# Optimization experiments

Hardware: AMD Instinct MI355X
Metric: run time of the kernel (lower is better)

The kernel has to match this reference:

```python
import jax, jax.numpy as jnp
from jax import lax
import numpy as np

# dims
N_ENT, M, K = 2048, 64, 32              # entities, mentions, candidates per mention
LT, LB, LM, LC, LD = 32, 128, 16, 128, 512  # char lengths: title, body, mention, context, doc
VOCAB, EMB = 5053, 300
H, HH, CCS, W = 256, 128, 512, 5        # hidden, per-dir LSTM hidden, char channels, conv width


def char_cnn(idx, emb, conv_w, conv_b):
    # Conv2d(1, CCS, [EMB, W]) applied to (N,1,EMB,L) == Conv1d(EMB, CCS, W); relu + max-pool over length
    x = jnp.swapaxes(emb[idx], 1, 2)                        # [N, EMB, L]
    y = lax.conv_general_dilated(x, conv_w, (1,), 'VALID')  # [N, CCS, L-W+1]
    return jax.nn.relu(y + conv_b[None, :, None]).max(axis=2)  # [N, CCS]


def _lstm_dir(x, Wih, Whh, bih, bhh):
    pre = x @ Wih.T + (bih + bhh)                            # [B, T, 4*HH]
    def step(carry, g_t):
        h, c = carry
        i, f, g, o = jnp.split(g_t + h @ Whh.T, 4, axis=-1)
        c = jax.nn.sigmoid(f) * c + jax.nn.sigmoid(i) * jnp.tanh(g)
        h = jax.nn.sigmoid(o) * jnp.tanh(c)
        return (h, c), h
    B = x.shape[0]
    z = jnp.zeros((B, Whh.shape[1]), x.dtype)
    _, hs = lax.scan(step, (z, z), jnp.swapaxes(pre, 0, 1))
    return jnp.swapaxes(hs, 0, 1)


def bilstm(x, Wih_f, Whh_f, bih_f, bhh_f, Wih_b, Whh_b, bih_b, bhh_b):
    fwd = _lstm_dir(x, Wih_f, Whh_f, bih_f, bhh_f)
    bwd = _lstm_dir(x[:, ::-1], Wih_b, Whh_b, bih_b, bhh_b)[:, ::-1]
    return jnp.concatenate([fwd, bwd], axis=-1)              # [B, T, H]


def att_flow(c, q, wc, bc, wq, bq, wcq, bcq):
    # BiDAF attention; c,q: [B,T,H] -> [B,T,4H]
    s = (c @ wc)[:, :, None] + (q @ wq)[:, None, :] \
        + jnp.einsum('bid,bjd,d->bij', c, q, wcq) + (bc + bq + bcq)
    a = jax.nn.softmax(s, axis=2)
    c2q = jnp.einsum('bij,bjd->bid', a, q)
    b = jax.nn.softmax(s.max(axis=2), axis=1)
    q2c = jnp.einsum('bi,bid->bd', b, c)[:, None, :]
    return jnp.concatenate([c, c2q, c * c2q, c * jnp.broadcast_to(q2c, c.shape)], axis=-1)


def setup_inputs() -> dict:
    key = jax.random.key(0)
    ks = jax.random.split(key, 16)
    rng = np.random.RandomState(0)
    # exactly K distinct candidate entities per mention (regularized mention_entity indicator)
    cand_idx = jnp.asarray(np.argsort(rng.rand(M, N_ENT), axis=1)[:, :K])
    emb = jax.random.uniform(ks[0], (VOCAB, EMB), jnp.float32, -0.001, 0.001).at[1].set(0.0)
    def rnd(k, shape, s=0.05):
        return jax.random.normal(k, shape, jnp.float32) * s
    return {
        'title_vec': jax.random.randint(ks[1], (N_ENT, LT), 0, VOCAB),
        'body_vec': jax.random.randint(ks[2], (N_ENT, LB), 0, VOCAB),
        'mention_vec': jax.random.randint(ks[3], (M, LM), 0, VOCAB),
        'context_vec': jax.random.randint(ks[4], (M, LC), 0, VOCAB),
        'doc_vec': jax.random.randint(ks[5], (LD,), 0, VOCAB),
        'cand_idx': cand_idx,
        'emb': emb,
        'conv_w': rnd(ks[6], (CCS, EMB, W), 0.02), 'conv_b': jnp.zeros((CCS,), jnp.float32),
        'Wih_f': rnd(ks[7], (4 * HH, CCS)), 'Whh_f': rnd(ks[8], (4 * HH, HH)),
        'bih_f': jnp.zeros((4 * HH,), jnp.float32), 'bhh_f': jnp.zeros((4 * HH,), jnp.float32),
        'Wih_b': rnd(ks[9], (4 * HH, CCS)), 'Whh_b': rnd(ks[10], (4 * HH, HH)),
        'bih_b': jnp.zeros((4 * HH,), jnp.float32), 'bhh_b': jnp.zeros((4 * HH,), jnp.float32),
        'wc': rnd(ks[11], (H,)), 'bc': jnp.zeros((), jnp.float32),
        'wq': rnd(ks[12], (H,)), 'bq': jnp.zeros((), jnp.float32),
        'wcq': rnd(ks[13], (H,)), 'bcq': jnp.zeros((), jnp.float32),
        'wz': rnd(ks[14], (4 * H,)), 'bz': jnp.zeros((), jnp.float32),
        'w_p1': jnp.asarray(0.7, jnp.float32), 'b_p1': jnp.asarray(0.1, jnp.float32),
        'w_p2': jnp.asarray(0.5, jnp.float32), 'b_p2': jnp.asarray(-0.1, jnp.float32),
    }


def reference(title_vec, body_vec, mention_vec, context_vec, doc_vec, cand_idx,
              emb, conv_w, conv_b,
              Wih_f, Whh_f, bih_f, bhh_f, Wih_b, Whh_b, bih_b, bhh_b,
              wc, bc, wq, bq, wcq, bcq, wz, bz, w_p1, b_p1, w_p2, b_p2):
    m, k = cand_idx.shape
    n = title_vec.shape[0]
    lstm_p = (Wih_f, Whh_f, bih_f, bhh_f, Wih_b, Whh_b, bih_b, bhh_b)
    # char-CNN features (compute once per unique sequence, then gather / broadcast)
    title_feat = char_cnn(title_vec, emb, conv_w, conv_b)         # [n, CCS]
    body_feat = char_cnn(body_vec, emb, conv_w, conv_b)           # [n, CCS]
    ctx_feat = char_cnn(context_vec, emb, conv_w, conv_b)         # [m, CCS]
    doc_feat = char_cnn(doc_vec[None], emb, conv_w, conv_b)[0]    # [CCS]
    # per-mention candidate sequences (seq dim = candidates, as in the original loop)
    title_h = bilstm(title_feat[cand_idx], *lstm_p)               # [m, k, H]
    body_h = bilstm(body_feat[cand_idx], *lstm_p)
    ctx_h = bilstm(jnp.broadcast_to(ctx_feat[:, None, :], (m, k, CCS)), *lstm_p)
    doc_h = bilstm(jnp.broadcast_to(doc_feat[None, None, :], (1, k, CCS)), *lstm_p)
    doc_h = jnp.broadcast_to(doc_h, (m, k, H))
    g = att_flow(ctx_h, title_h, wc, bc, wq, bq, wcq, bcq)        # [m, k, 4H]
    h = att_flow(doc_h, body_h, wc, bc, wq, bq, wcq, bcq)
    p1 = g @ wz + bz                                              # [m, k]
    p2 = h @ wz + bz
    score = w_p1 * p1 + b_p1 + w_p2 * p2 + b_p2
    # len(true_output)==1 branch is always taken in the original: raw scores, softmax, sum-normalized
    score_sm = jax.nn.softmax(score, axis=1)
    score_un = score / score.sum(axis=1, keepdims=True)
    rows = jnp.arange(m)[:, None]
    def scatter(v):
        return jnp.zeros((m, n), v.dtype).at[rows, cand_idx].set(v)
    return scatter(score), scatter(score_sm), scatter(score_un)
```

## Files before the change

kernel.cpp:

```cpp
#include <hip/hip_runtime.h>
#include <hip/hip_fp16.h>
#include <math.h>

#define DEDUP_B 34439168ULL
#define AH_B    34459648ULL
#define BH_B    37695488ULL
#define BHP_B   39333888ULL
#define WHH_B   40382464ULL
#define AHP_B   34459648ULL

typedef _Float16 half8 __attribute__((ext_vector_type(8)));
typedef float f32x4 __attribute__((ext_vector_type(4)));

__device__ inline void add8(float* a, float4 r){
  const __half2* h = (const __half2*)&r;
  #pragma unroll
  for (int q = 0; q < 4; ++q){
    float2 f = __half22float2(h[q]);
    a[2*q]   += f.x;
    a[2*q+1] += f.y;
  }
}

__global__ __launch_bounds__(256) void k_prep(unsigned int* __restrict__ out32, int n,
                                              unsigned int* __restrict__ dd32,
                                              float* __restrict__ featDoc,
                                              const float* __restrict__ emb, _Float16* __restrict__ A_h,
                                              const float* __restrict__ convw, _Float16* __restrict__ B_h,
                                              const float* __restrict__ WihF, const float* __restrict__ WihB,
                                              _Float16* __restrict__ B_hp,
                                              const float* __restrict__ WhhF, const float* __restrict__ WhhB,
                                              _Float16* __restrict__ WhhH){
  const long o0 = n;
  const long o1 = o0 + 2112;
  const long o2 = o1 + 512;
  const long o3 = o2 + 1617920;
  const long o4 = o3 + 819200;
  const long o5 = o4 + 524288;
  const long o6 = o5 + 131072;
  for (long t = (long)blockIdx.x * 256 + threadIdx.x; t < o6; t += (long)gridDim.x * 256){
    if (t < o0){
      out32[t] = 0u;
    } else if (t < o1){
      dd32[t - o0] = 0u;
    } else if (t < o2){
      featDoc[t - o1] = 0.f;
    } else if (t < o3){
      long u = t - o2;
      int row = (int)(u / 320), col = (int)(u - (long)row * 320);
      float v = (row < 5053 && col < 300) ? emb[(size_t)row * 300 + col] * 1024.f : 0.f;
      A_h[u] = (_Float16)v;
    } else if (t < o4){
      long u = t - o3;
      int nn = (int)(u / 320), k = (int)(u - (long)nn * 320);
      int w = nn >> 9, c = nn & 511;
      float v = (k < 300) ? convw[((size_t)c * 300 + k) * 5 + w] : 0.f;
      B_h[u] = (_Float16)v;
    } else if (t < o5){
      long u = t - o4;
      int dir = (int)(u >> 18), r = (int)(u & 262143);
      B_hp[u] = (_Float16)((dir ? WihB : WihF)[r]);
    } else {
      long u = t - o5;
      int dir = (int)(u >> 16), r = (int)(u & 65535);
      WhhH[u] = (_Float16)((dir ? WhhB : WhhF)[r]);
    }
  }
}

__global__ __launch_bounds__(256) void k_mark(const int* __restrict__ cand, int* __restrict__ flags){
  int t = blockIdx.x * 256 + threadIdx.x;
  flags[cand[t]] = 1;
}

__global__ __launch_bounds__(256) void k_compact(const int* __restrict__ flags,
                                                 int* __restrict__ nUsed, int* __restrict__ list){
  int t = blockIdx.x * 256 + threadIdx.x;
  if (flags[t]){
    int s = atomicAdd(nUsed, 1);
    list[s] = t;
  }
}

__global__ __launch_bounds__(256) void k_contrib(const _Float16* __restrict__ A_h,
                                                 const _Float16* __restrict__ B_h,
                                                 __half* __restrict__ contrib){
  int tid = threadIdx.x;
  int lane = tid & 63, wid = tid >> 6;
  int wr = wid >> 1, wc = wid & 1;
  int m0 = blockIdx.x * 64 + wr * 32;
  int n0 = blockIdx.y * 128 + wc * 64;
  int lr = lane & 15, lk = (lane >> 4) * 8;

  const _Float16* Ap = A_h + (size_t)(m0 + lr) * 320 + lk;
  const _Float16* Bp = B_h + (size_t)(n0 + lr) * 320 + lk;

  f32x4 acc[2][4];
  #pragma unroll
  for (int fr = 0; fr < 2; ++fr)
    #pragma unroll
    for (int fc = 0; fc < 4; ++fc) acc[fr][fc] = (f32x4){0.f, 0.f, 0.f, 0.f};

  for (int kk = 0; kk < 320; kk += 32){
    half8 a0 = *(const half8*)(Ap + kk);
    half8 a1 = *(const half8*)(Ap + 16 * 320 + kk);
    half8 b0 = *(const half8*)(Bp + kk);
    half8 b1 = *(const half8*)(Bp + 16 * 320 + kk);
    half8 b2 = *(const half8*)(Bp + 32 * 320 + kk);
    half8 b3 = *(const half8*)(Bp + 48 * 320 + kk);
    acc[0][0] = __builtin_amdgcn_mfma_f32_16x16x32_f16(a0, b0, acc[0][0], 0, 0, 0);
    acc[0][1] = __builtin_amdgcn_mfma_f32_16x16x32_f16(a0, b1, acc[0][1], 0, 0, 0);
    acc[0][2] = __builtin_amdgcn_mfma_f32_16x16x32_f16(a0, b2, acc[0][2], 0, 0, 0);
    acc[0][3] = __builtin_amdgcn_mfma_f32_16x16x32_f16(a0, b3, acc[0][3], 0, 0, 0);
    acc[1][0] = __builtin_amdgcn_mfma_f32_16x16x32_f16(a1, b0, acc[1][0], 0, 0, 0);
    acc[1][1] = __builtin_amdgcn_mfma_f32_16x16x32_f16(a1, b1, acc[1][1], 0, 0, 0);
    acc[1][2] = __builtin_amdgcn_mfma_f32_16x16x32_f16(a1, b2, acc[1][2], 0, 0, 0);
    acc[1][3] = __builtin_amdgcn_mfma_f32_16x16x32_f16(a1, b3, acc[1][3], 0, 0, 0);
  }
  const float s = 1.f / 1024.f;
  #pragma unroll
  for (int fr = 0; fr < 2; ++fr){
    int row = m0 + fr * 16 + (lane >> 4) * 4;
    #pragma unroll
    for (int fc = 0; fc < 4; ++fc){
      int col = n0 + fc * 16 + lr;
      #pragma unroll
      for (int r = 0; r < 4; ++r)
        contrib[(size_t)(row + r) * 2560 + col] = __float2half(acc[fr][fc][r] * s);
    }
  }
}

__global__ __launch_bounds__(256) void k_conv(const int* __restrict__ title_v,
                                              const int* __restrict__ body_v,
                                              const int* __restrict__ ctx_v,
                                              const __half* __restrict__ contrib,
                                              const float* __restrict__ convb,
                                              float* __restrict__ featAll,
                                              const int* __restrict__ list,
                                              const int* __restrict__ nUsed){
  __shared__ int tok[128];
  __shared__ float red[256 * 9];
  int bg = blockIdx.x, tid = threadIdx.x;
  const int* idx; int L, row0; bool useList;
  if (bg < 16384){ idx = title_v; L = 32;  row0 = 0;    useList = true; }
  else if (bg < 32768){ bg -= 16384; idx = body_v; L = 128; row0 = 2048; useList = true; }
  else { bg -= 32768; idx = ctx_v; L = 128; row0 = 4096; useList = false; }
  int g = bg & 7, sIdx = bg >> 3;
  int s = sIdx;
  if (useList){
    if (sIdx >= *nUsed) return;
    s = list[sIdx];
  }
  const int* row = idx + (size_t)s * L;
  for (int i = tid; i < L; i += 256) tok[i] = row[i];
  __syncthreads();
  int c8 = tid & 7;
  int pg = tid >> 3;
  int cOff = g * 64 + c8 * 8;
  float bias[8], mx[8];
  {
    float4 b0 = *(const float4*)(convb + cOff);
    float4 b1 = *(const float4*)(convb + cOff + 4);
    bias[0]=b0.x; bias[1]=b0.y; bias[2]=b0.z; bias[3]=b0.w;
    bias[4]=b1.x; bias[5]=b1.y; bias[6]=b1.z; bias[7]=b1.w;
  }
  #pragma unroll
  for (int k = 0; k < 8; ++k) mx[k] = 0.f;
  int P = L - 4;
  int per = (P + 31) >> 5;
  int p = pg * per, pe = min(p + per, P);
  for (; p + 1 < pe; p += 2){
    float a0[8], a1[8];
    #pragma unroll
    for (int k = 0; k < 8; ++k){ a0[k] = bias[k]; a1[k] = bias[k]; }
    #pragma unroll
    for (int w = 0; w < 5; ++w){
      float4 r0 = *(const float4*)(contrib + ((size_t)tok[p + w] * 5 + w) * 512 + cOff);
      float4 r1 = *(const float4*)(contrib + ((size_t)tok[p + 1 + w] * 5 + w) * 512 + cOff);
      add8(a0, r0);
      add8(a1, r1);
    }
    #pragma unroll
    for (int k = 0; k < 8; ++k) mx[k] = fmaxf(mx[k], fmaxf(a0[k], a1[k]));
  }
  if (p < pe){
    float a0[8];
    #pragma unroll
    for (int k = 0; k < 8; ++k) a0[k] = bias[k];
    #pragma unroll
    for (int w = 0; w < 5; ++w){
      float4 r0 = *(const float4*)(contrib + ((size_t)tok[p + w] * 5 + w) * 512 + cOff);
      add8(a0, r0);
    }
    #pragma unroll
    for (int k = 0; k < 8; ++k) mx[k] = fmaxf(mx[k], a0[k]);
  }
  #pragma unroll
  for (int k = 0; k < 8; ++k) red[tid * 9 + k] = mx[k];
  __syncthreads();
  if (tid < 64){
    int c8r = tid >> 3, kr = tid & 7;
    float o = red[c8r * 9 + kr];
    #pragma unroll
    for (int q = 1; q < 32; ++q)
      o = fmaxf(o, red[(q * 8 + c8r) * 9 + kr]);
    featAll[(size_t)(row0 + s) * 512 + g * 64 + tid] = o;
  }
}

__global__ __launch_bounds__(256) void k_conv_doc(const int* __restrict__ doc,
                                                  const __half* __restrict__ contrib,
                                                  const float* __restrict__ convb,
                                                  float* __restrict__ featDoc){
  __shared__ int tok[512];
  __shared__ float red[256 * 9];
  int b = blockIdx.x, tid = threadIdx.x;
  for (int i = tid; i < 512; i += 256) tok[i] = doc[i];
  __syncthreads();
  int c8 = tid & 63, pg = tid >> 6;
  float bias[8], mx[8];
  {
    float4 b0 = *(const float4*)(convb + c8 * 8);
    float4 b1 = *(const float4*)(convb + c8 * 8 + 4);
    bias[0]=b0.x; bias[1]=b0.y; bias[2]=b0.z; bias[3]=b0.w;
    bias[4]=b1.x; bias[5]=b1.y; bias[6]=b1.z; bias[7]=b1.w;
  }
  #pragma unroll
  for (int k = 0; k < 8; ++k) mx[k] = 0.f;
  int p0 = b * 16, p1 = min(p0 + 16, 508);
  int n = p1 - p0;
  int per = (n + 3) >> 2;
  int p = p0 + pg * per, pe = min(p + per, p1);
  for (; p < pe; ++p){
    float a0[8];
    #pragma unroll
    for (int k = 0; k < 8; ++k) a0[k] = bias[k];
    #pragma unroll
    for (int w = 0; w < 5; ++w){
      float4 r0 = *(const float4*)(contrib + ((size_t)tok[p + w] * 5 + w) * 512 + c8 * 8);
      add8(a0, r0);
    }
    #pragma unroll
    for (int k = 0; k < 8; ++k) mx[k] = fmaxf(mx[k], a0[k]);
  }
  #pragma unroll
  for (int k = 0; k < 8; ++k) red[tid * 9 + k] = mx[k];
  __syncthreads();
  if (tid < 64){
    #pragma unroll
    for (int k = 0; k < 8; ++k){
      float o = fmaxf(fmaxf(red[tid * 9 + k], red[(tid + 64) * 9 + k]),
                      fmaxf(red[(tid + 128) * 9 + k], red[(tid + 192) * 9 + k]));
      atomicMax((int*)(featDoc + tid * 8 + k), __float_as_int(o));
    }
  }
}

__global__ __launch_bounds__(256) void k_featH(const float* __restrict__ feat, _Float16* __restrict__ A_hp){
  int t = blockIdx.x * 256 + threadIdx.x;
  if (t >= 4224 * 512) return;
  int row = t >> 9;
  float v = (row < 4161) ? feat[t] * 1024.f : 0.f;
  A_hp[t] = (_Float16)v;
}

__global__ __launch_bounds__(256) void k_proj(const _Float16* __restrict__ A_hp,
                                              const _Float16* __restrict__ B_hp,
                                              const float* __restrict__ bihF, const float* __restrict__ bhhF,
                                              const float* __restrict__ bihB, const float* __restrict__ bhhB,
                                              float* __restrict__ preAll){
  int tid = threadIdx.x;
  int lane = tid & 63, wid = tid >> 6;
  int wr = wid >> 1, wc = wid & 1;
  int dir = blockIdx.z;
  int m0 = blockIdx.x * 64 + wr * 32;
  int n0 = blockIdx.y * 128 + wc * 64;
  int lr = lane & 15, lk = (lane >> 4) * 8;

  const _Float16* Ap = A_hp + (size_t)(m0 + lr) * 512 + lk;
  const _Float16* Bp = B_hp + (size_t)dir * 262144 + (size_t)(n0 + lr) * 512 + lk;

  f32x4 acc[2][4];
  #pragma unroll
  for (int fr = 0; fr < 2; ++fr)
    #pragma unroll
    for (int fc = 0; fc < 4; ++fc) acc[fr][fc] = (f32x4){0.f, 0.f, 0.f, 0.f};

  for (int kk = 0; kk < 512; kk += 32){
    half8 a0 = *(const half8*)(Ap + kk);
    half8 a1 = *(const half8*)(Ap + 16 * 512 + kk);
    half8 b0 = *(const half8*)(Bp + kk);
    half8 b1 = *(const half8*)(Bp + 16 * 512 + kk);
    half8 b2 = *(const half8*)(Bp + 32 * 512 + kk);
    half8 b3 = *(const half8*)(Bp + 48 * 512 + kk);
    acc[0][0] = __builtin_amdgcn_mfma_f32_16x16x32_f16(a0, b0, acc[0][0], 0, 0, 0);
    acc[0][1] = __builtin_amdgcn_mfma_f32_16x16x32_f16(a0, b1, acc[0][1], 0, 0, 0);
    acc[0][2] = __builtin_amdgcn_mfma_f32_16x16x32_f16(a0, b2, acc[0][2], 0, 0, 0);
    acc[0][3] = __builtin_amdgcn_mfma_f32_16x16x32_f16(a0, b3, acc[0][3], 0, 0, 0);
    acc[1][0] = __builtin_amdgcn_mfma_f32_16x16x32_f16(a1, b0, acc[1][0], 0, 0, 0);
    acc[1][1] = __builtin_amdgcn_mfma_f32_16x16x32_f16(a1, b1, acc[1][1], 0, 0, 0);
    acc[1][2] = __builtin_amdgcn_mfma_f32_16x16x32_f16(a1, b2, acc[1][2], 0, 0, 0);
    acc[1][3] = __builtin_amdgcn_mfma_f32_16x16x32_f16(a1, b3, acc[1][3], 0, 0, 0);
  }
  const float s = 1.f / 1024.f;
  const float* bih = dir ? bihB : bihF;
  const float* bhh = dir ? bhhB : bhhF;
  float* outp = preAll + (size_t)dir * 4176 * 512;
  #pragma unroll
  for (int fr = 0; fr < 2; ++fr){
    int row = m0 + fr * 16 + (lane >> 4) * 4;
    #pragma unroll
    for (int fc = 0; fc < 4; ++fc){
      int col = n0 + fc * 16 + lr;
      float bias = bih[col] + bhh[col];
      #pragma unroll
      for (int r = 0; r < 4; ++r)
        if (row + r < 4176)
          outp[(size_t)(row + r) * 512 + col] = acc[fr][fc][r] * s + bias;
    }
  }
}

__global__ __launch_bounds__(512, 2) void k_recur(const float* __restrict__ preAll,
                                                  const _Float16* __restrict__ WhhH,
                                                  const int* __restrict__ cand,
                                                  float* __restrict__ hT, float* __restrict__ hB,
                                                  float* __restrict__ hC, float* __restrict__ hD){
  int c = blockIdx.x, dir = blockIdx.y, tid = threadIdx.x;
  int lstm = (c < 64) ? 0 : (c < 128) ? 1 : (c < 192) ? 2 : 3;
  int b = (lstm == 3) ? 0 : (c - lstm * 64);
  const float* pre = preAll + (size_t)dir * 4176 * 512;
  float* hout;
  if (lstm == 0)      hout = hT + (size_t)b * 32 * 256;
  else if (lstm == 1) hout = hB + (size_t)b * 32 * 256;
  else if (lstm == 2) hout = hC + (size_t)b * 32 * 256;
  else                hout = hD;
  hout += dir * 128;

  int cidx = tid >> 2;
  int kc = tid & 3;
  int k0 = kc * 32;

  half8 wv[4][4];
  #pragma unroll
  for (int m = 0; m < 4; ++m){
    const _Float16* wp = WhhH + (size_t)dir * 65536 + (size_t)(m * 128 + cidx) * 128 + k0;
    #pragma unroll
    for (int j = 0; j < 4; ++j)
      wv[m][j] = *(const half8*)(wp + j * 8);
  }
  {
    float* wf = (float*)wv;
    #pragma unroll
    for (int i = 0; i < 64; ++i)
      asm volatile("v_mov_b32 %0, %1" : "=v"(wf[i]) : "v"(wf[i]));
  }

  __shared__ __align__(16) float hpad[2][4][36];
  __shared__ int candL[32];
  if (tid < 288) ((float*)hpad)[tid] = 0.f;
  if (lstm < 2 && tid < 32) candL[tid] = cand[b * 32 + tid];
  __syncthreads();

  float pf;
  {
    int t0 = dir ? 31 : 0;
    int rowi;
    if (lstm == 0)      rowi = candL[t0];
    else if (lstm == 1) rowi = 2048 + candL[t0];
    else if (lstm == 2) rowi = 4096 + b;
    else                rowi = 4160;
    pf = pre[(size_t)rowi * 512 + kc * 128 + cidx];
  }

  float cst = 0.f;
  for (int s = 0; s < 32; ++s){
    int t = dir ? (31 - s) : s;
    int cur = s & 1, nxt = cur ^ 1;
    float pfn = 0.f;
    if (s < 31){
      int t2 = dir ? (31 - (s + 1)) : (s + 1);
      int rowi;
      if (lstm == 0)      rowi = candL[t2];
      else if (lstm == 1) rowi = 2048 + candL[t2];
      else if (lstm == 2) rowi = 4096 + b;
      else                rowi = 4160;
      pfn = pre[(size_t)rowi * 512 + kc * 128 + cidx];
    }
    float p0 = 0.f, p1 = 0.f, p2 = 0.f, p3 = 0.f;
    #pragma unroll
    for (int j = 0; j < 4; ++j){
      float4 ha = *(const float4*)&hpad[cur][kc][j * 8];
      float4 hb = *(const float4*)&hpad[cur][kc][j * 8 + 4];
      p0 += (float)wv[0][j][0] * ha.x + (float)wv[0][j][1] * ha.y
          + (float)wv[0][j][2] * ha.z + (float)wv[0][j][3] * ha.w
          + (float)wv[0][j][4] * hb.x + (float)wv[0][j][5] * hb.y
          + (float)wv[0][j][6] * hb.z + (float)wv[0][j][7] * hb.w;
      p1 += (float)wv[1][j][0] * ha.x + (float)wv[1][j][1] * ha.y
          + (float)wv[1][j][2] * ha.z + (float)wv[1][j][3] * ha.w
          + (float)wv[1][j][4] * hb.x + (float)wv[1][j][5] * hb.y
          + (float)wv[1][j][6] * hb.z + (float)wv[1][j][7] * hb.w;
      p2 += (float)wv[2][j][0] * ha.x + (float)wv[2][j][1] * ha.y
          + (float)wv[2][j][2] * ha.z + (float)wv[2][j][3] * ha.w
          + (float)wv[2][j][4] * hb.x + (float)wv[2][j][5] * hb.y
          + (float)wv[2][j][6] * hb.z + (float)wv[2][j][7] * hb.w;
      p3 += (float)wv[3][j][0] * ha.x + (float)wv[3][j][1] * ha.y
          + (float)wv[3][j][2] * ha.z + (float)wv[3][j][3] * ha.w
          + (float)wv[3][j][4] * hb.x + (float)wv[3][j][5] * hb.y
          + (float)wv[3][j][6] * hb.z + (float)wv[3][j][7] * hb.w;
    }
    p0 += __shfl_xor(p0, 1); p0 += __shfl_xor(p0, 2);
    p1 += __shfl_xor(p1, 1); p1 += __shfl_xor(p1, 2);
    p2 += __shfl_xor(p2, 1); p2 += __shfl_xor(p2, 2);
    p3 += __shfl_xor(p3, 1); p3 += __shfl_xor(p3, 2);
    float g = (kc == 0) ? p0 : (kc == 1) ? p1 : (kc == 2) ? p2 : p3;
    g += pf;
    float av = (kc == 2) ? tanhf(g) : 1.f / (1.f + __expf(-g));
    float a1 = __shfl_xor(av, 1);
    float a2 = __shfl_xor(av, 2);
    float a3 = __shfl_xor(av, 3);
    if (kc == 0){
      cst = a1 * cst + av * a2;
      float hf = a3 * tanhf(cst);
      hpad[nxt][cidx >> 5][cidx & 31] = hf;
      hout[(size_t)t * 256 + cidx] = hf;
    }
    pf = pfn;
    __syncthreads();
  }
}

__global__ __launch_bounds__(256) void k_att1(const float* __restrict__ hC,
                                              const float* __restrict__ hT,
                                              const float* __restrict__ hD,
                                              const float* __restrict__ hB,
                                              const float* __restrict__ wc_g, const float* __restrict__ bc_g,
                                              const float* __restrict__ wq_g, const float* __restrict__ bq_g,
                                              const float* __restrict__ wcq_g, const float* __restrict__ bcq_g,
                                              const float* __restrict__ wz_g, const float* __restrict__ bz_g,
                                              double* __restrict__ pOut){
  int b = blockIdx.x, pass = blockIdx.y, tid = threadIdx.x;
  __shared__ float cS[32][260];
  __shared__ float qS[32][260];
  __shared__ float wS[7][256];
  __shared__ double q2cS[256];
  __shared__ double cwS[32], qwS[32], qzS[32], paS[32], smaxS[32], bsmS[32];
  const float* cp = pass ? hD : (hC + (size_t)b * 8192);
  const float* qp = (pass ? hB : hT) + (size_t)b * 8192;
  for (int k = tid; k < 2048; k += 256){
    int i = k >> 6, d4 = (k & 63) * 4;
    *(float4*)&cS[i][d4] = *(const float4*)(cp + i * 256 + d4);
    *(float4*)&qS[i][d4] = *(const float4*)(qp + i * 256 + d4);
  }
  wS[0][tid] = wc_g[tid];
  wS[1][tid] = wq_g[tid];
  wS[2][tid] = wcq_g[tid];
  wS[3][tid] = wz_g[tid];
  wS[4][tid] = wz_g[256 + tid];
  wS[5][tid] = wz_g[512 + tid];
  wS[6][tid] = wz_g[768 + tid];
  __syncthreads();
  int i = tid >> 3, js = tid & 7;
  {
    double a = 0, aq = 0, az = 0;
    for (int k = 0; k < 32; ++k){
      int d = js * 32 + k;
      a  += (double)cS[i][d] * (double)wS[0][d];
      aq += (double)qS[i][d] * (double)wS[1][d];
      az += (double)qS[i][d] * (double)wS[4][d];
    }
    #pragma unroll
    for (int m = 1; m < 8; m <<= 1){
      a  += __shfl_xor(a, m);
      aq += __shfl_xor(aq, m);
      az += __shfl_xor(az, m);
    }
    if (js == 0){ cwS[i] = a; qwS[i] = aq; qzS[i] = az; }
  }
  __syncthreads();
  double bsum = (double)bc_g[0] + (double)bq_g[0] + (double)bcq_g[0];
  double sa[4] = {0,0,0,0}, ta[4] = {0,0,0,0};
  for (int d = 0; d < 256; ++d){
    double cd = (double)cS[i][d];
    double cw1 = cd * (double)wS[2][d];
    double cw2 = cd * (double)wS[5][d];
    #pragma unroll
    for (int m = 0; m < 4; ++m){
      double qv = (double)qS[js + m * 8][d];
      sa[m] += cw1 * qv;
      ta[m] += cw2 * qv;
    }
  }
  {
    double cwv = cwS[i];
    double s[4], mx = -1e300;
    #pragma unroll
    for (int m = 0; m < 4; ++m){
      s[m] = sa[m] + cwv + qwS[js + m * 8] + bsum;
      mx = fmax(mx, s[m]);
    }
    #pragma unroll
    for (int m = 1; m < 8; m <<= 1) mx = fmax(mx, __shfl_xor(mx, m));
    double esum = 0, eacc = 0;
    #pragma unroll
    for (int m = 0; m < 4; ++m){
      double e = exp(s[m] - mx);
      esum += e;
      eacc += e * (qzS[js + m * 8] + ta[m]);
    }
    #pragma unroll
    for (int m = 1; m < 8; m <<= 1){
      esum += __shfl_xor(esum, m);
      eacc += __shfl_xor(eacc, m);
    }
    if (js == 0){ paS[i] = eacc / esum; smaxS[i] = mx; }
  }
  __syncthreads();
  if (tid < 32){
    double v = smaxS[tid];
    double m2 = v;
    #pragma unroll
    for (int m = 1; m < 32; m <<= 1) m2 = fmax(m2, __shfl_xor(m2, m));
    double e = exp(v - m2), ssum = e;
    #pragma unroll
    for (int m = 1; m < 32; m <<= 1) ssum += __shfl_xor(ssum, m);
    bsmS[tid] = e / ssum;
  }
  __syncthreads();
  {
    double a = 0;
    for (int ii = 0; ii < 32; ++ii) a += bsmS[ii] * (double)cS[ii][tid];
    q2cS[tid] = a;
  }
  __syncthreads();
  {
    double t1 = 0, t4 = 0;
    for (int k = 0; k < 32; ++k){
      int d = js * 32 + k;
      double cd = (double)cS[i][d];
      t1 += cd * (double)wS[3][d];
      t4 += cd * q2cS[d] * (double)wS[6][d];
    }
    #pragma unroll
    for (int m = 1; m < 8; m <<= 1){
      t1 += __shfl_xor(t1, m);
      t4 += __shfl_xor(t4, m);
    }
    if (js == 0)
      pOut[((size_t)pass * 64 + b) * 32 + i] = t1 + paS[i] + t4 + (double)bz_g[0];
  }
}

__global__ __launch_bounds__(64) void k_att2(const double* __restrict__ pOut,
                                             const float* __restrict__ wp1_g, const float* __restrict__ bp1_g,
                                             const float* __restrict__ wp2_g, const float* __restrict__ bp2_g,
                                             const int* __restrict__ cand,
                                             float* __restrict__ out){
  int b = blockIdx.x, tid = threadIdx.x;
  if (tid >= 32) return;
  double p1 = pOut[(size_t)b * 32 + tid];
  double p2 = pOut[(size_t)(64 + b) * 32 + tid];
  double sc = (double)wp1_g[0] * p1 + (double)bp1_g[0]
            + (double)wp2_g[0] * p2 + (double)bp2_g[0];
  double mx = sc, rs = sc;
  #pragma unroll
  for (int m = 1; m < 32; m <<= 1){
    mx = fmax(mx, __shfl_xor(mx, m));
    rs += __shfl_xor(rs, m);
  }
  double e = exp(sc - mx), es = e;
  #pragma unroll
  for (int m = 1; m < 32; m <<= 1) es += __shfl_xor(es, m);
  int col = cand[b * 32 + tid];
  out[(size_t)b * 2048 + col] = (float)sc;
  out[131072 + (size_t)b * 2048 + col] = (float)(e / es);
  out[262144 + (size_t)b * 2048 + col] = (float)(sc / rs);
}

extern "C" void kernel_launch(void* const* d_in, const int* in_sizes, int n_in,
                              void* d_out, int out_size, void* d_ws, size_t ws_size,
                              hipStream_t stream) {
  const int* title_v = (const int*)d_in[0];
  const int* body_v  = (const int*)d_in[1];
  const int* ctx_v   = (const int*)d_in[3];
  const int* doc_v   = (const int*)d_in[4];
  const int* cand    = (const int*)d_in[5];
  const float* emb   = (const float*)d_in[6];
  const float* convw = (const float*)d_in[7];
  const float* convb = (const float*)d_in[8];
  const float* WihF  = (const float*)d_in[9];
  const float* WhhF  = (const float*)d_in[10];
  const float* bihF  = (const float*)d_in[11];
  const float* bhhF  = (const float*)d_in[12];
  const float* WihB  = (const float*)d_in[13];
  const float* WhhB  = (const float*)d_in[14];
  const float* bihB  = (const float*)d_in[15];
  const float* bhhB  = (const float*)d_in[16];
  float* out = (float*)d_out;

  const size_t CONTRIB_B = (size_t)5056 * 2560 * 2;
  char* base = (char*)d_ws;
  if (ws_size < 60325888) return;
  __half* contrib = (__half*)base;
  char* featBase = base + CONTRIB_B;
  float* feat = (float*)featBase;
  float* featDoc = feat + (size_t)4160 * 512;

  int* flags = (int*)(base + DEDUP_B);
  int* nUsed = (int*)(base + DEDUP_B + 8192);
  int* list  = (int*)(base + DEDUP_B + 8448);

  _Float16* A_h  = (_Float16*)(base + AH_B);
  _Float16* B_h  = (_Float16*)(base + BH_B);
  _Float16* A_hp = (_Float16*)(base + AHP_B);
  _Float16* B_hp = (_Float16*)(base + BHP_B);
  _Float16* WhhH = (_Float16*)(base + WHH_B);

  float*  preAll = (float*)(base + 2097152);
  float*  hT     = (float*)(base + 19202048);
  float*  hB     = (float*)(base + 21299200);
  float*  hC     = (float*)(base + 23396352);
  float*  hD     = (float*)(base + 25493504);
  double* pOut   = (double*)(base + 25526272);

  k_prep<<<4096, 256, 0, stream>>>((unsigned int*)out, out_size,
                                   (unsigned int*)(base + DEDUP_B), featDoc,
                                   emb, A_h, convw, B_h, WihF, WihB, B_hp,
                                   WhhF, WhhB, WhhH);
  k_mark<<<8, 256, 0, stream>>>(cand, flags);
  k_compact<<<8, 256, 0, stream>>>(flags, nUsed, list);
  k_contrib<<<dim3(79, 20), 256, 0, stream>>>(A_h, B_h, contrib);

  k_conv<<<33280, 256, 0, stream>>>(title_v, body_v, ctx_v, contrib, convb, feat, list, nUsed);
  k_conv_doc<<<32, 256, 0, stream>>>(doc_v, contrib, convb, featDoc);

  k_featH<<<8448, 256, 0, stream>>>(feat, A_hp);
  k_proj<<<dim3(66, 4, 2), 256, 0, stream>>>(A_hp, B_hp, bihF, bhhF, bihB, bhhB, preAll);
  k_recur<<<dim3(193, 2), 512, 0, stream>>>(preAll, WhhH, cand, hT, hB, hC, hD);
  k_att1<<<dim3(64, 2), 256, 0, stream>>>(hC, hT, hD, hB,
                                (const float*)d_in[17], (const float*)d_in[18],
                                (const float*)d_in[19], (const float*)d_in[20],
                                (const float*)d_in[21], (const float*)d_in[22],
                                (const float*)d_in[23], (const float*)d_in[24],
                                pOut);
  k_att2<<<64, 64, 0, stream>>>(pOut,
                                (const float*)d_in[25], (const float*)d_in[26],
                                (const float*)d_in[27], (const float*)d_in[28],
                                cand, out);
}
```

Measured before the change: 367.4 us.

## Fuse dedup kernels, merge doc conv into k_conv, write fp16 features directly

Replaces the separate mark and compact kernels with one single-block kernel that keeps flags in shared memory, so the global flag buffer and its zeroing go away. The document char-CNN blocks are appended to the main k_conv grid, and k_conv now writes its pooled features straight into the fp16, pre-scaled projection input. This drops the intermediate fp32 feature buffer and the separate k_featH conversion pass. The aim is fewer launches and less global memory traffic, at the cost of a small extra tail kernel and more branching inside k_conv.

```diff
diff --git a/kernel.cpp b/kernel.cpp
--- a/kernel.cpp
+++ b/kernel.cpp
@@ -23,7 +23,6 @@
 }
 
 __global__ __launch_bounds__(256) void k_prep(unsigned int* __restrict__ out32, int n,
-                                              unsigned int* __restrict__ dd32,
                                               float* __restrict__ featDoc,
                                               const float* __restrict__ emb, _Float16* __restrict__ A_h,
                                               const float* __restrict__ convw, _Float16* __restrict__ B_h,
@@ -32,54 +31,61 @@
                                               const float* __restrict__ WhhF, const float* __restrict__ WhhB,
                                               _Float16* __restrict__ WhhH){
   const long o0 = n;
-  const long o1 = o0 + 2112;
-  const long o2 = o1 + 512;
-  const long o3 = o2 + 1617920;
-  const long o4 = o3 + 819200;
-  const long o5 = o4 + 524288;
-  const long o6 = o5 + 131072;
-  for (long t = (long)blockIdx.x * 256 + threadIdx.x; t < o6; t += (long)gridDim.x * 256){
+  const long o1 = o0 + 512;
+  const long o2 = o1 + 1617920;
+  const long o3 = o2 + 819200;
+  const long o4 = o3 + 524288;
+  const long o5 = o4 + 131072;
+  for (long t = (long)blockIdx.x * 256 + threadIdx.x; t < o5; t += (long)gridDim.x * 256){
     if (t < o0){
       out32[t] = 0u;
     } else if (t < o1){
-      dd32[t - o0] = 0u;
+      featDoc[t - o0] = 0.f;
     } else if (t < o2){
-      featDoc[t - o1] = 0.f;
-    } else if (t < o3){
-      long u = t - o2;
+      long u = t - o1;
       int row = (int)(u / 320), col = (int)(u - (long)row * 320);
       float v = (row < 5053 && col < 300) ? emb[(size_t)row * 300 + col] * 1024.f : 0.f;
       A_h[u] = (_Float16)v;
-    } else if (t < o4){
-      long u = t - o3;
+    } else if (t < o3){
+      long u = t - o2;
       int nn = (int)(u / 320), k = (int)(u - (long)nn * 320);
       int w = nn >> 9, c = nn & 511;
       float v = (k < 300) ? convw[((size_t)c * 300 + k) * 5 + w] : 0.f;
       B_h[u] = (_Float16)v;
-    } else if (t < o5){
-      long u = t - o4;
+    } else if (t < o4){
+      long u = t - o3;
       int dir = (int)(u >> 18), r = (int)(u & 262143);
       B_hp[u] = (_Float16)((dir ? WihB : WihF)[r]);
     } else {
-      long u = t - o5;
+      long u = t - o4;
       int dir = (int)(u >> 16), r = (int)(u & 65535);
       WhhH[u] = (_Float16)((dir ? WhhB : WhhF)[r]);
     }
   }
 }
 
-__global__ __launch_bounds__(256) void k_mark(const int* __restrict__ cand, int* __restrict__ flags){
-  int t = blockIdx.x * 256 + threadIdx.x;
-  flags[cand[t]] = 1;
-}
-
-__global__ __launch_bounds__(256) void k_compact(const int* __restrict__ flags,
-                                                 int* __restrict__ nUsed, int* __restrict__ list){
-  int t = blockIdx.x * 256 + threadIdx.x;
-  if (flags[t]){
-    int s = atomicAdd(nUsed, 1);
-    list[s] = t;
-  }
+__global__ __launch_bounds__(1024) void k_markcompact(const int* __restrict__ cand,
+                                                      int* __restrict__ nUsed,
+                                                      int* __restrict__ list){
+  __shared__ int flags[2048];
+  __shared__ int cnt;
+  int tid = threadIdx.x;
+  flags[tid] = 0; flags[tid + 1024] = 0;
+  if (tid == 0) cnt = 0;
+  __syncthreads();
+  flags[cand[tid]] = 1;
+  flags[cand[tid + 1024]] = 1;
+  __syncthreads();
+  #pragma unroll
+  for (int q = 0; q < 2; ++q){
+    int e = tid + q * 1024;
+    if (flags[e]){
+      int s = atomicAdd(&cnt, 1);
+      list[s] = e;
+    }
+  }
+  __syncthreads();
+  if (tid == 0) *nUsed = cnt;
 }
 
 __global__ __launch_bounds__(256) void k_contrib(const _Float16* __restrict__ A_h,
@@ -134,14 +140,61 @@
 __global__ __launch_bounds__(256) void k_conv(const int* __restrict__ title_v,
                                               const int* __restrict__ body_v,
                                               const int* __restrict__ ctx_v,
+                                              const int* __restrict__ doc_v,
                                               const __half* __restrict__ contrib,
                                               const float* __restrict__ convb,
-                                              float* __restrict__ featAll,
+                                              _Float16* __restrict__ A_hp,
+                                              float* __restrict__ featDoc,
                                               const int* __restrict__ list,
                                               const int* __restrict__ nUsed){
-  __shared__ int tok[128];
+  __shared__ int tok[512];
   __shared__ float red[256 * 9];
   int bg = blockIdx.x, tid = threadIdx.x;
+
+  if (bg >= 33280){
+    int b = bg - 33280;
+    for (int i = tid; i < 512; i += 256) tok[i] = doc_v[i];
+    __syncthreads();
+    int c8 = tid & 63, pg = tid >> 6;
+    float bias[8], mx[8];
+    {
+      float4 b0 = *(const float4*)(convb + c8 * 8);
+      float4 b1 = *(const float4*)(convb + c8 * 8 + 4);
+      bias[0]=b0.x; bias[1]=b0.y; bias[2]=b0.z; bias[3]=b0.w;
+      bias[4]=b1.x; bias[5]=b1.y; bias[6]=b1.z; bias[7]=b1.w;
+    }
+    #pragma unroll
+    for (int k = 0; k < 8; ++k) mx[k] = 0.f;
+    int p0 = b * 16, p1 = min(p0 + 16, 508);
+    int n = p1 - p0;
+    int per = (n + 3) >> 2;
+    int p = p0 + pg * per, pe = min(p + per, p1);
+    for (; p < pe; ++p){
+      float a0[8];
+      #pragma unroll
+      for (int k = 0; k < 8; ++k) a0[k] = bias[k];
+      #pragma unroll
+      for (int w = 0; w < 5; ++w){
+        float4 r0 = *(const float4*)(contrib + ((size_t)tok[p + w] * 5 + w) * 512 + c8 * 8);
+        add8(a0, r0);
+      }
+      #pragma unroll
+      for (int k = 0; k < 8; ++k) mx[k] = fmaxf(mx[k], a0[k]);
+    }
+    #pragma unroll
+    for (int k = 0; k < 8; ++k) red[tid * 9 + k] = mx[k];
+    __syncthreads();
+    if (tid < 64){
+      #pragma unroll
+      for (int k = 0; k < 8; ++k){
+        float o = fmaxf(fmaxf(red[tid * 9 + k], red[(tid + 64) * 9 + k]),
+                        fmaxf(red[(tid + 128) * 9 + k], red[(tid + 192) * 9 + k]));
+        atomicMax((int*)(featDoc + tid * 8 + k), __float_as_int(o));
+      }
+    }
+    return;
+  }
+
   const int* idx; int L, row0; bool useList;
   if (bg < 16384){ idx = title_v; L = 32;  row0 = 0;    useList = true; }
   else if (bg < 32768){ bg -= 16384; idx = body_v; L = 128; row0 = 2048; useList = true; }
@@ -205,64 +258,17 @@
     #pragma unroll
     for (int q = 1; q < 32; ++q)
       o = fmaxf(o, red[(q * 8 + c8r) * 9 + kr]);
-    featAll[(size_t)(row0 + s) * 512 + g * 64 + tid] = o;
-  }
-}
-
-__global__ __launch_bounds__(256) void k_conv_doc(const int* __restrict__ doc,
-                                                  const __half* __restrict__ contrib,
-                                                  const float* __restrict__ convb,
-                                                  float* __restrict__ featDoc){
-  __shared__ int tok[512];
-  __shared__ float red[256 * 9];
-  int b = blockIdx.x, tid = threadIdx.x;
-  for (int i = tid; i < 512; i += 256) tok[i] = doc[i];
-  __syncthreads();
-  int c8 = tid & 63, pg = tid >> 6;
-  float bias[8], mx[8];
-  {
-    float4 b0 = *(const float4*)(convb + c8 * 8);
-    float4 b1 = *(const float4*)(convb + c8 * 8 + 4);
-    bias[0]=b0.x; bias[1]=b0.y; bias[2]=b0.z; bias[3]=b0.w;
-    bias[4]=b1.x; bias[5]=b1.y; bias[6]=b1.z; bias[7]=b1.w;
-  }
-  #pragma unroll
-  for (int k = 0; k < 8; ++k) mx[k] = 0.f;
-  int p0 = b * 16, p1 = min(p0 + 16, 508);
-  int n = p1 - p0;
-  int per = (n + 3) >> 2;
-  int p = p0 + pg * per, pe = min(p + per, p1);
-  for (; p < pe; ++p){
-    float a0[8];
-    #pragma unroll
-    for (int k = 0; k < 8; ++k) a0[k] = bias[k];
-    #pragma unroll
-    for (int w = 0; w < 5; ++w){
-      float4 r0 = *(const float4*)(contrib + ((size_t)tok[p + w] * 5 + w) * 512 + c8 * 8);
-      add8(a0, r0);
-    }
-    #pragma unroll
-    for (int k = 0; k < 8; ++k) mx[k] = fmaxf(mx[k], a0[k]);
-  }
-  #pragma unroll
-  for (int k = 0; k < 8; ++k) red[tid * 9 + k] = mx[k];
-  __syncthreads();
-  if (tid < 64){
-    #pragma unroll
-    for (int k = 0; k < 8; ++k){
-      float o = fmaxf(fmaxf(red[tid * 9 + k], red[(tid + 64) * 9 + k]),
-                      fmaxf(red[(tid + 128) * 9 + k], red[(tid + 192) * 9 + k]));
-      atomicMax((int*)(featDoc + tid * 8 + k), __float_as_int(o));
-    }
-  }
-}
-
-__global__ __launch_bounds__(256) void k_featH(const float* __restrict__ feat, _Float16* __restrict__ A_hp){
+    A_hp[(size_t)(row0 + s) * 512 + g * 64 + tid] = (_Float16)(o * 1024.f);
+  }
+}
+
+__global__ __launch_bounds__(256) void k_featTail(const float* __restrict__ featDoc,
+                                                  _Float16* __restrict__ A_hp){
   int t = blockIdx.x * 256 + threadIdx.x;
-  if (t >= 4224 * 512) return;
-  int row = t >> 9;
-  float v = (row < 4161) ? feat[t] * 1024.f : 0.f;
-  A_hp[t] = (_Float16)v;
+  if (t < 512)
+    A_hp[(size_t)4160 * 512 + t] = (_Float16)(featDoc[t] * 1024.f);
+  else
+    A_hp[(size_t)4160 * 512 + t] = (_Float16)0.f;
 }
 
 __global__ __launch_bounds__(256) void k_proj(const _Float16* __restrict__ A_hp,
@@ -603,13 +609,10 @@
   char* base = (char*)d_ws;
   if (ws_size < 60325888) return;
   __half* contrib = (__half*)base;
-  char* featBase = base + CONTRIB_B;
-  float* feat = (float*)featBase;
-  float* featDoc = feat + (size_t)4160 * 512;
-
-  int* flags = (int*)(base + DEDUP_B);
-  int* nUsed = (int*)(base + DEDUP_B + 8192);
-  int* list  = (int*)(base + DEDUP_B + 8448);
+  float* featDoc = (float*)(base + CONTRIB_B + (size_t)4160 * 512 * 4);
+
+  int* nUsed = (int*)(base + DEDUP_B);
+  int* list  = (int*)(base + DEDUP_B + 256);
 
   _Float16* A_h  = (_Float16*)(base + AH_B);
   _Float16* B_h  = (_Float16*)(base + BH_B);
@@ -624,18 +627,16 @@
   float*  hD     = (float*)(base + 25493504);
   double* pOut   = (double*)(base + 25526272);
 
-  k_prep<<<4096, 256, 0, stream>>>((unsigned int*)out, out_size,
-                                   (unsigned int*)(base + DEDUP_B), featDoc,
+  k_prep<<<4096, 256, 0, stream>>>((unsigned int*)out, out_size, featDoc,
                                    emb, A_h, convw, B_h, WihF, WihB, B_hp,
                                    WhhF, WhhB, WhhH);
-  k_mark<<<8, 256, 0, stream>>>(cand, flags);
-  k_compact<<<8, 256, 0, stream>>>(flags, nUsed, list);
+  k_markcompact<<<1, 1024, 0, stream>>>(cand, nUsed, list);
   k_contrib<<<dim3(79, 20), 256, 0, stream>>>(A_h, B_h, contrib);
 
-  k_conv<<<33280, 256, 0, stream>>>(title_v, body_v, ctx_v, contrib, convb, feat, list, nUsed);
-  k_conv_doc<<<32, 256, 0, stream>>>(doc_v, contrib, convb, featDoc);
-
-  k_featH<<<8448, 256, 0, stream>>>(feat, A_hp);
+  k_conv<<<33312, 256, 0, stream>>>(title_v, body_v, ctx_v, doc_v, contrib, convb,
+                                    A_hp, featDoc, list, nUsed);
+  k_featTail<<<128, 256, 0, stream>>>(featDoc, A_hp);
+
   k_proj<<<dim3(66, 4, 2), 256, 0, stream>>>(A_hp, B_hp, bihF, bhhF, bihB, bhhB, preAll);
   k_recur<<<dim3(193, 2), 512, 0, stream>>>(preAll, WhhH, cand, hT, hB, hC, hD);
   k_att1<<<dim3(64, 2), 256, 0, stream>>>(hC, hT, hD, hB,
```

Measured after the change: 354.0 us. -3.6%, faster.
